# Kernel tuning notes

Hardware: AMD Instinct MI355X
Metric: run time of the kernel (lower is better)

## Reference

```python
import jax, jax.numpy as jnp
import numpy as np

NF = 256  # node_feat_size
GF = 256  # graph_feat_size
V = 262144
G = 4096


def setup_inputs() -> dict:
    key = jax.random.key(0)
    ks = jax.random.split(key, 12)
    node_feats = jax.random.normal(ks[0], (V, NF), dtype=jnp.float32)
    g_feats = jax.random.normal(ks[1], (G, GF), dtype=jnp.float32)
    segment_ids = jnp.sort(jax.random.randint(ks[2], (V,), 0, G, dtype=jnp.int32))
    s = 0.05
    # compute_logits: Linear(NF+GF -> 1)
    Wl = jax.random.normal(ks[3], (1, NF + GF), dtype=jnp.float32) * s
    bl = jnp.zeros((1,), dtype=jnp.float32)
    # project_nodes: Linear(NF -> GF)  (dropout=0 -> identity)
    Wp = jax.random.normal(ks[4], (GF, NF), dtype=jnp.float32) * s
    bp = jnp.zeros((GF,), dtype=jnp.float32)
    # GRUCell(GF, GF), torch gate order (r, z, n)
    W_ih = jax.random.normal(ks[5], (3 * GF, GF), dtype=jnp.float32) * s
    W_hh = jax.random.normal(ks[6], (3 * GF, GF), dtype=jnp.float32) * s
    b_ih = jnp.zeros((3 * GF,), dtype=jnp.float32)
    b_hh = jnp.zeros((3 * GF,), dtype=jnp.float32)
    return dict(node_feats=node_feats, g_feats=g_feats, segment_ids=segment_ids,
                Wl=Wl, bl=bl, Wp=Wp, bp=bp,
                W_ih=W_ih, W_hh=W_hh, b_ih=b_ih, b_hh=b_hh)


def reference(node_feats, g_feats, segment_ids, Wl, bl, Wp, bp, W_ih, W_hh, b_ih, b_hh):
    num_graphs = g_feats.shape[0]
    # broadcast relu(g_feats) to nodes, concat with node feats, logits Linear + LeakyReLU
    gb = jax.nn.relu(g_feats)[segment_ids]                      # [V, GF]
    cat = jnp.concatenate([gb, node_feats], axis=1)             # [V, GF+NF]
    z = jax.nn.leaky_relu(cat @ Wl.T + bl, negative_slope=0.01) # [V, 1]
    # segmented softmax over nodes per graph
    m = jax.ops.segment_max(z, segment_ids, num_segments=num_graphs,
                            indices_are_sorted=True)            # [G, 1]
    e = jnp.exp(z - m[segment_ids])                             # [V, 1]
    denom = jax.ops.segment_sum(e, segment_ids, num_segments=num_graphs,
                                indices_are_sorted=True)        # [G, 1]
    a = e / denom[segment_ids]                                  # [V, 1]
    # project nodes (dropout p=0 -> identity) and weighted sum per graph
    hv = node_feats @ Wp.T + bp                                 # [V, GF]
    context = jax.ops.segment_sum(a * hv, segment_ids, num_segments=num_graphs,
                                  indices_are_sorted=True)      # [G, GF]
    context = jax.nn.elu(context)
    # GRUCell: input=context, hidden=g_feats, torch gate order r,z,n
    gi = context @ W_ih.T + b_ih                                # [G, 3*GF]
    gh = g_feats @ W_hh.T + b_hh                                # [G, 3*GF]
    i_r, i_z, i_n = jnp.split(gi, 3, axis=1)
    h_r, h_z, h_n = jnp.split(gh, 3, axis=1)
    r = jax.nn.sigmoid(i_r + h_r)
    u = jax.nn.sigmoid(i_z + h_z)
    n = jnp.tanh(i_n + r * h_n)
    h_new = (1.0 - u) * n + u * g_feats
    return h_new
```

## Files before the change

### kernel.cpp

```cpp
#include <hip/hip_runtime.h>
#include <hip/hip_bf16.h>
#include <stdint.h>

typedef unsigned short u16;
typedef __attribute__((ext_vector_type(8))) short short8;
typedef __attribute__((ext_vector_type(4))) float floatx4;

#define NFEAT 256

__device__ __forceinline__ unsigned short f2b(float f) {
    unsigned int x = __builtin_bit_cast(unsigned int, f);
    x += 0x7fffu + ((x >> 16) & 1u);
    return (unsigned short)(x >> 16);
}
__device__ __forceinline__ float sigmoidf_(float x) {
    return 1.0f / (1.0f + __expf(-x));
}

__global__ void __launch_bounds__(256)
k1_attn_pool(const float* __restrict__ nf, const float* __restrict__ gf,
             const int* __restrict__ seg, const float* __restrict__ Wl,
             const float* __restrict__ bl,
             const float* __restrict__ Wp, const float* __restrict__ Wih,
             const float* __restrict__ Whh,
             u16* __restrict__ s_out,
             float* __restrict__ pres, u16* __restrict__ gfb,
             u16* __restrict__ wpb, u16* __restrict__ wihb, u16* __restrict__ whhb,
             int V)
{
    const int g = blockIdx.x;
    const int t = threadIdx.x;
    __shared__ float red[256];
    __shared__ float accs[4][256];
    __shared__ float mws[4], lws[4];

    {
        const int n1 = 256 * 256;
        const int n2 = n1 + 768 * 256;
        const int n3 = n2 + 768 * 256;
        int idx = g * 256 + t;
        if (idx < n3) {
            if (idx < n1)       wpb[idx]       = f2b(Wp[idx]);
            else if (idx < n2)  wihb[idx - n1] = f2b(Wih[idx - n1]);
            else                whhb[idx - n2] = f2b(Whh[idx - n2]);
        }
    }

    const float gfv = gf[(size_t)g * NFEAT + t];
    gfb[(size_t)g * NFEAT + t] = f2b(gfv);
    red[t] = fmaxf(gfv, 0.0f) * Wl[t];
    __syncthreads();
    #pragma unroll
    for (int off = 128; off > 0; off >>= 1) {
        if (t < off) red[t] += red[t + off];
        __syncthreads();
    }
    const float gbase = red[0] + bl[0];
    __syncthreads();

    int lo = 0, hi = V;
    while (lo < hi) { int mid = (lo + hi) >> 1; if (seg[mid] < g) lo = mid + 1; else hi = mid; }
    const int start = lo;
    hi = V;
    while (lo < hi) { int mid = (lo + hi) >> 1; if (seg[mid] <= g) lo = mid + 1; else hi = mid; }
    const int count = lo - start;

    const int lane = t & 63;
    const int wv = t >> 6;

    const float4 wn = *(const float4*)(Wl + NFEAT + lane * 4);

    float m = -3.0e38f, l = 0.0f;
    float4 acc = {0.f, 0.f, 0.f, 0.f};
    const float* base = nf + (size_t)start * NFEAT + lane * 4;

    float4 x = {0.f, 0.f, 0.f, 0.f};
    if (wv < count) x = *(const float4*)(base + (size_t)wv * NFEAT);
    for (int i = wv; i < count; i += 4) {
        float4 nx = {0.f, 0.f, 0.f, 0.f};
        if (i + 4 < count) nx = *(const float4*)(base + (size_t)(i + 4) * NFEAT);
        float d = x.x * wn.x + x.y * wn.y + x.z * wn.z + x.w * wn.w;
        #pragma unroll
        for (int off = 32; off > 0; off >>= 1) d += __shfl_xor(d, off);
        float z = d + gbase;
        z = (z > 0.0f) ? z : 0.01f * z;
        float mn = fmaxf(m, z);
        float c = __expf(m - mn);
        float p = __expf(z - mn);
        l = l * c + p;
        acc.x = acc.x * c + p * x.x;
        acc.y = acc.y * c + p * x.y;
        acc.z = acc.z * c + p * x.z;
        acc.w = acc.w * c + p * x.w;
        m = mn;
        x = nx;
    }

    accs[wv][lane * 4 + 0] = acc.x;
    accs[wv][lane * 4 + 1] = acc.y;
    accs[wv][lane * 4 + 2] = acc.z;
    accs[wv][lane * 4 + 3] = acc.w;
    if (lane == 0) { mws[wv] = m; lws[wv] = l; }
    __syncthreads();

    const float M = fmaxf(fmaxf(mws[0], mws[1]), fmaxf(mws[2], mws[3]));
    const float c0 = __expf(mws[0] - M), c1 = __expf(mws[1] - M);
    const float c2 = __expf(mws[2] - M), c3 = __expf(mws[3] - M);
    const float L = lws[0] * c0 + lws[1] * c1 + lws[2] * c2 + lws[3] * c3;
    const float sv = accs[0][t] * c0 + accs[1][t] * c1 + accs[2][t] * c2 + accs[3][t] * c3;
    const float inv = (L > 0.0f) ? 1.0f / L : 0.0f;
    s_out[(size_t)g * NFEAT + t] = f2b(sv * inv);
    if (t == 0) pres[g] = (count > 0) ? 1.0f : 0.0f;
}

__global__ void __launch_bounds__(256)
k2a_project(const u16* __restrict__ s, const u16* __restrict__ Wpb,
            const float* __restrict__ bp, const float* __restrict__ pres,
            u16* __restrict__ ctx)
{
    const int t = threadIdx.x;
    const int wid = blockIdx.x * 4 + (t >> 6);
    const int lane = t & 63;
    const int m0 = (wid >> 4) * 16;
    const int n0 = (wid & 15) * 16;
    const int lr = lane & 15;
    const int kh = lane >> 4;

    const short* A = (const short*)s   + (size_t)(m0 + lr) * NFEAT + kh * 8;
    const short* B = (const short*)Wpb + (size_t)(n0 + lr) * NFEAT + kh * 8;

    floatx4 acc = {0.f, 0.f, 0.f, 0.f};
    #pragma unroll
    for (int k = 0; k < NFEAT; k += 32) {
        short8 a = *(const short8*)(A + k);
        short8 b = *(const short8*)(B + k);
        acc = __builtin_amdgcn_mfma_f32_16x16x32_bf16(a, b, acc, 0, 0, 0);
    }
    const int col = n0 + lr;
    const float bias = bp[col];
    const int rbase = m0 + kh * 4;
    #pragma unroll
    for (int r = 0; r < 4; ++r) {
        int row = rbase + r;
        float x = acc[r] + bias * pres[row];
        x = (x > 0.0f) ? x : (__expf(x) - 1.0f);
        ctx[(size_t)row * NFEAT + col] = f2b(x);
    }
}

__global__ void __launch_bounds__(256)
k2b_gru(const u16* __restrict__ ctx, const u16* __restrict__ gfb,
        const float* __restrict__ gf,
        const u16* __restrict__ Wih, const u16* __restrict__ Whh,
        const float* __restrict__ bih, const float* __restrict__ bhh,
        float* __restrict__ out)
{
    const int t = threadIdx.x;
    const int wid = blockIdx.x * 4 + (t >> 6);
    const int lane = t & 63;
    const int m0 = (wid >> 4) * 16;
    const int j0 = (wid & 15) * 16;
    const int lr = lane & 15;
    const int kh = lane >> 4;

    const short* A1 = (const short*)ctx + (size_t)(m0 + lr) * NFEAT + kh * 8;
    const short* A2 = (const short*)gfb + (size_t)(m0 + lr) * NFEAT + kh * 8;
    const size_t boff = (size_t)(j0 + lr) * NFEAT + kh * 8;
    const short* Bir = (const short*)Wih + boff;
    const short* Biz = Bir + 256 * NFEAT;
    const short* Bin = Bir + 512 * NFEAT;
    const short* Bhr = (const short*)Whh + boff;
    const short* Bhz = Bhr + 256 * NFEAT;
    const short* Bhn = Bhr + 512 * NFEAT;

    floatx4 air = {0,0,0,0}, aiz = {0,0,0,0}, ain = {0,0,0,0};
    floatx4 ahr = {0,0,0,0}, ahz = {0,0,0,0}, ahn = {0,0,0,0};
    #pragma unroll
    for (int k = 0; k < NFEAT; k += 32) {
        short8 a1 = *(const short8*)(A1 + k);
        short8 a2 = *(const short8*)(A2 + k);
        air = __builtin_amdgcn_mfma_f32_16x16x32_bf16(a1, *(const short8*)(Bir + k), air, 0, 0, 0);
        aiz = __builtin_amdgcn_mfma_f32_16x16x32_bf16(a1, *(const short8*)(Biz + k), aiz, 0, 0, 0);
        ain = __builtin_amdgcn_mfma_f32_16x16x32_bf16(a1, *(const short8*)(Bin + k), ain, 0, 0, 0);
        ahr = __builtin_amdgcn_mfma_f32_16x16x32_bf16(a2, *(const short8*)(Bhr + k), ahr, 0, 0, 0);
        ahz = __builtin_amdgcn_mfma_f32_16x16x32_bf16(a2, *(const short8*)(Bhz + k), ahz, 0, 0, 0);
        ahn = __builtin_amdgcn_mfma_f32_16x16x32_bf16(a2, *(const short8*)(Bhn + k), ahn, 0, 0, 0);
    }
    const int col = j0 + lr;
    const float b_ir = bih[col], b_iz = bih[256 + col], b_in = bih[512 + col];
    const float b_hr = bhh[col], b_hz = bhh[256 + col], b_hn = bhh[512 + col];
    const int rbase = m0 + kh * 4;
    #pragma unroll
    for (int r = 0; r < 4; ++r) {
        int row = rbase + r;
        float rg = sigmoidf_((air[r] + b_ir) + (ahr[r] + b_hr));
        float ug = sigmoidf_((aiz[r] + b_iz) + (ahz[r] + b_hz));
        float ng = tanhf((ain[r] + b_in) + rg * (ahn[r] + b_hn));
        float h  = gf[(size_t)row * NFEAT + col];
        out[(size_t)row * NFEAT + col] = (1.0f - ug) * ng + ug * h;
    }
}

extern "C" void kernel_launch(void* const* d_in, const int* in_sizes, int n_in,
                              void* d_out, int out_size, void* d_ws, size_t ws_size,
                              hipStream_t stream)
{
    const float* nf  = (const float*)d_in[0];
    const float* gf  = (const float*)d_in[1];
    const int*   seg = (const int*)d_in[2];
    const float* Wl  = (const float*)d_in[3];
    const float* bl  = (const float*)d_in[4];
    const float* Wp  = (const float*)d_in[5];
    const float* bp  = (const float*)d_in[6];
    const float* Wih = (const float*)d_in[7];
    const float* Whh = (const float*)d_in[8];
    const float* bih = (const float*)d_in[9];
    const float* bhh = (const float*)d_in[10];

    const int V = in_sizes[2];
    const int G = in_sizes[1] / NFEAT;

    char* ws = (char*)d_ws;
    u16*   sbuf = (u16*)ws;                           ws += (size_t)G * NFEAT * 2;
    u16*   ctx  = (u16*)ws;                           ws += (size_t)G * NFEAT * 2;
    u16*   gfb  = (u16*)ws;                           ws += (size_t)G * NFEAT * 2;
    u16*   wpb  = (u16*)ws;                           ws += (size_t)256 * 256 * 2;
    u16*   wihb = (u16*)ws;                           ws += (size_t)768 * 256 * 2;
    u16*   whhb = (u16*)ws;                           ws += (size_t)768 * 256 * 2;
    float* pres = (float*)ws;                         ws += (size_t)G * 4;

    k1_attn_pool<<<G, 256, 0, stream>>>(nf, gf, seg, Wl, bl, Wp, Wih, Whh,
                                        sbuf, pres, gfb, wpb, wihb, whhb, V);
    k2a_project<<<G / 4, 256, 0, stream>>>(sbuf, wpb, bp, pres, ctx);
    k2b_gru<<<G / 4, 256, 0, stream>>>(ctx, gfb, gf, wihb, whhb, bih, bhh, (float*)d_out);
    (void)ws_size; (void)n_in; (void)out_size;
}
```

Before: 438.1 us.

## Fuse projection and GRU kernels via LDS context; unroll pooling loop by two nodes

Merges the projection+ELU kernel and the GRU kernel into one 512-thread kernel per 16 graphs. The context tile stays in shared memory instead of round-tripping through global memory, and A fragments are kept in registers and reused across two output tiles per wave. Separately, the attention-pooling loop now handles two nodes per wave per iteration, which raises memory-level parallelism in the dominant streaming pass. The cost is higher register pressure and fewer blocks in the fused GEMM stage.

```diff
diff --git a/kernel.cpp b/kernel.cpp
--- a/kernel.cpp
+++ b/kernel.cpp
@@ -74,26 +74,39 @@
     float4 acc = {0.f, 0.f, 0.f, 0.f};
     const float* base = nf + (size_t)start * NFEAT + lane * 4;
 
-    float4 x = {0.f, 0.f, 0.f, 0.f};
-    if (wv < count) x = *(const float4*)(base + (size_t)wv * NFEAT);
-    for (int i = wv; i < count; i += 4) {
-        float4 nx = {0.f, 0.f, 0.f, 0.f};
-        if (i + 4 < count) nx = *(const float4*)(base + (size_t)(i + 4) * NFEAT);
-        float d = x.x * wn.x + x.y * wn.y + x.z * wn.z + x.w * wn.w;
-        #pragma unroll
-        for (int off = 32; off > 0; off >>= 1) d += __shfl_xor(d, off);
-        float z = d + gbase;
-        z = (z > 0.0f) ? z : 0.01f * z;
-        float mn = fmaxf(m, z);
-        float c = __expf(m - mn);
-        float p = __expf(z - mn);
-        l = l * c + p;
-        acc.x = acc.x * c + p * x.x;
-        acc.y = acc.y * c + p * x.y;
-        acc.z = acc.z * c + p * x.z;
-        acc.w = acc.w * c + p * x.w;
+    float4 x0 = {0.f,0.f,0.f,0.f}, x1 = {0.f,0.f,0.f,0.f};
+    {
+        int i = wv * 2;
+        if (i < count)     x0 = *(const float4*)(base + (size_t)i * NFEAT);
+        if (i + 1 < count) x1 = *(const float4*)(base + (size_t)(i + 1) * NFEAT);
+    }
+    for (int i = wv * 2; i < count; i += 8) {
+        float4 p0v = {0.f,0.f,0.f,0.f}, p1v = {0.f,0.f,0.f,0.f};
+        if (i + 8 < count) p0v = *(const float4*)(base + (size_t)(i + 8) * NFEAT);
+        if (i + 9 < count) p1v = *(const float4*)(base + (size_t)(i + 9) * NFEAT);
+
+        float d0 = x0.x * wn.x + x0.y * wn.y + x0.z * wn.z + x0.w * wn.w;
+        float d1 = x1.x * wn.x + x1.y * wn.y + x1.z * wn.z + x1.w * wn.w;
+        #pragma unroll
+        for (int off = 32; off > 0; off >>= 1) {
+            d0 += __shfl_xor(d0, off);
+            d1 += __shfl_xor(d1, off);
+        }
+        float z0 = d0 + gbase; z0 = (z0 > 0.0f) ? z0 : 0.01f * z0;
+        float z1 = d1 + gbase; z1 = (z1 > 0.0f) ? z1 : 0.01f * z1;
+        if (i + 1 >= count) z1 = -3.0e38f;
+
+        float mn = fmaxf(m, fmaxf(z0, z1));
+        float c  = __expf(m - mn);
+        float p0 = __expf(z0 - mn);
+        float p1 = __expf(z1 - mn);
+        l = l * c + p0 + p1;
+        acc.x = acc.x * c + p0 * x0.x + p1 * x1.x;
+        acc.y = acc.y * c + p0 * x0.y + p1 * x1.y;
+        acc.z = acc.z * c + p0 * x0.z + p1 * x1.z;
+        acc.w = acc.w * c + p0 * x0.w + p1 * x1.w;
         m = mn;
-        x = nx;
+        x0 = p0v; x1 = p1v;
     }
 
     accs[wv][lane * 4 + 0] = acc.x;
@@ -113,91 +126,95 @@
     if (t == 0) pres[g] = (count > 0) ? 1.0f : 0.0f;
 }
 
-__global__ void __launch_bounds__(256)
-k2a_project(const u16* __restrict__ s, const u16* __restrict__ Wpb,
-            const float* __restrict__ bp, const float* __restrict__ pres,
-            u16* __restrict__ ctx)
+#define CTX_LD 264
+__global__ void __launch_bounds__(512)
+k2_fused(const u16* __restrict__ s, const u16* __restrict__ wpb,
+         const float* __restrict__ bp, const float* __restrict__ pres,
+         const u16* __restrict__ gfb, const float* __restrict__ gf,
+         const u16* __restrict__ wihb, const u16* __restrict__ whhb,
+         const float* __restrict__ bih, const float* __restrict__ bhh,
+         float* __restrict__ out)
 {
+    __shared__ u16 ctx[16][CTX_LD];
     const int t = threadIdx.x;
-    const int wid = blockIdx.x * 4 + (t >> 6);
+    const int w = t >> 6;
     const int lane = t & 63;
-    const int m0 = (wid >> 4) * 16;
-    const int n0 = (wid & 15) * 16;
+    const int m0 = blockIdx.x * 16;
     const int lr = lane & 15;
     const int kh = lane >> 4;
 
-    const short* A = (const short*)s   + (size_t)(m0 + lr) * NFEAT + kh * 8;
-    const short* B = (const short*)Wpb + (size_t)(n0 + lr) * NFEAT + kh * 8;
-
-    floatx4 acc = {0.f, 0.f, 0.f, 0.f};
+    {
+        const short* A = (const short*)s + (size_t)(m0 + lr) * NFEAT + kh * 8;
+        short8 af[8];
+        #pragma unroll
+        for (int kk = 0; kk < 8; ++kk) af[kk] = *(const short8*)(A + kk * 32);
+
+        #pragma unroll
+        for (int nt = 0; nt < 2; ++nt) {
+            const int n0 = (w * 2 + nt) * 16;
+            const short* B = (const short*)wpb + (size_t)(n0 + lr) * NFEAT + kh * 8;
+            floatx4 acc = {0.f, 0.f, 0.f, 0.f};
+            #pragma unroll
+            for (int kk = 0; kk < 8; ++kk)
+                acc = __builtin_amdgcn_mfma_f32_16x16x32_bf16(af[kk], *(const short8*)(B + kk * 32), acc, 0, 0, 0);
+            const int col = n0 + lr;
+            const float bias = bp[col];
+            #pragma unroll
+            for (int r = 0; r < 4; ++r) {
+                int rl = kh * 4 + r;
+                float x = acc[r] + bias * pres[m0 + rl];
+                x = (x > 0.0f) ? x : (__expf(x) - 1.0f);
+                ctx[rl][col] = f2b(x);
+            }
+        }
+    }
+    __syncthreads();
+
+    short8 a1[8], a2[8];
     #pragma unroll
-    for (int k = 0; k < NFEAT; k += 32) {
-        short8 a = *(const short8*)(A + k);
-        short8 b = *(const short8*)(B + k);
-        acc = __builtin_amdgcn_mfma_f32_16x16x32_bf16(a, b, acc, 0, 0, 0);
-    }
-    const int col = n0 + lr;
-    const float bias = bp[col];
-    const int rbase = m0 + kh * 4;
+    for (int kk = 0; kk < 8; ++kk)
+        a1[kk] = *(const short8*)&ctx[lr][kk * 32 + kh * 8];
+    {
+        const short* A2 = (const short*)gfb + (size_t)(m0 + lr) * NFEAT + kh * 8;
+        #pragma unroll
+        for (int kk = 0; kk < 8; ++kk) a2[kk] = *(const short8*)(A2 + kk * 32);
+    }
+
     #pragma unroll
-    for (int r = 0; r < 4; ++r) {
-        int row = rbase + r;
-        float x = acc[r] + bias * pres[row];
-        x = (x > 0.0f) ? x : (__expf(x) - 1.0f);
-        ctx[(size_t)row * NFEAT + col] = f2b(x);
-    }
-}
-
-__global__ void __launch_bounds__(256)
-k2b_gru(const u16* __restrict__ ctx, const u16* __restrict__ gfb,
-        const float* __restrict__ gf,
-        const u16* __restrict__ Wih, const u16* __restrict__ Whh,
-        const float* __restrict__ bih, const float* __restrict__ bhh,
-        float* __restrict__ out)
-{
-    const int t = threadIdx.x;
-    const int wid = blockIdx.x * 4 + (t >> 6);
-    const int lane = t & 63;
-    const int m0 = (wid >> 4) * 16;
-    const int j0 = (wid & 15) * 16;
-    const int lr = lane & 15;
-    const int kh = lane >> 4;
-
-    const short* A1 = (const short*)ctx + (size_t)(m0 + lr) * NFEAT + kh * 8;
-    const short* A2 = (const short*)gfb + (size_t)(m0 + lr) * NFEAT + kh * 8;
-    const size_t boff = (size_t)(j0 + lr) * NFEAT + kh * 8;
-    const short* Bir = (const short*)Wih + boff;
-    const short* Biz = Bir + 256 * NFEAT;
-    const short* Bin = Bir + 512 * NFEAT;
-    const short* Bhr = (const short*)Whh + boff;
-    const short* Bhz = Bhr + 256 * NFEAT;
-    const short* Bhn = Bhr + 512 * NFEAT;
-
-    floatx4 air = {0,0,0,0}, aiz = {0,0,0,0}, ain = {0,0,0,0};
-    floatx4 ahr = {0,0,0,0}, ahz = {0,0,0,0}, ahn = {0,0,0,0};
-    #pragma unroll
-    for (int k = 0; k < NFEAT; k += 32) {
-        short8 a1 = *(const short8*)(A1 + k);
-        short8 a2 = *(const short8*)(A2 + k);
-        air = __builtin_amdgcn_mfma_f32_16x16x32_bf16(a1, *(const short8*)(Bir + k), air, 0, 0, 0);
-        aiz = __builtin_amdgcn_mfma_f32_16x16x32_bf16(a1, *(const short8*)(Biz + k), aiz, 0, 0, 0);
-        ain = __builtin_amdgcn_mfma_f32_16x16x32_bf16(a1, *(const short8*)(Bin + k), ain, 0, 0, 0);
-        ahr = __builtin_amdgcn_mfma_f32_16x16x32_bf16(a2, *(const short8*)(Bhr + k), ahr, 0, 0, 0);
-        ahz = __builtin_amdgcn_mfma_f32_16x16x32_bf16(a2, *(const short8*)(Bhz + k), ahz, 0, 0, 0);
-        ahn = __builtin_amdgcn_mfma_f32_16x16x32_bf16(a2, *(const short8*)(Bhn + k), ahn, 0, 0, 0);
-    }
-    const int col = j0 + lr;
-    const float b_ir = bih[col], b_iz = bih[256 + col], b_in = bih[512 + col];
-    const float b_hr = bhh[col], b_hz = bhh[256 + col], b_hn = bhh[512 + col];
-    const int rbase = m0 + kh * 4;
-    #pragma unroll
-    for (int r = 0; r < 4; ++r) {
-        int row = rbase + r;
-        float rg = sigmoidf_((air[r] + b_ir) + (ahr[r] + b_hr));
-        float ug = sigmoidf_((aiz[r] + b_iz) + (ahz[r] + b_hz));
-        float ng = tanhf((ain[r] + b_in) + rg * (ahn[r] + b_hn));
-        float h  = gf[(size_t)row * NFEAT + col];
-        out[(size_t)row * NFEAT + col] = (1.0f - ug) * ng + ug * h;
+    for (int jt = 0; jt < 2; ++jt) {
+        const int j0 = (w * 2 + jt) * 16;
+        const size_t boff = (size_t)(j0 + lr) * NFEAT + kh * 8;
+        const short* Bir = (const short*)wihb + boff;
+        const short* Biz = Bir + 256 * NFEAT;
+        const short* Bin = Bir + 512 * NFEAT;
+        const short* Bhr = (const short*)whhb + boff;
+        const short* Bhz = Bhr + 256 * NFEAT;
+        const short* Bhn = Bhr + 512 * NFEAT;
+
+        floatx4 air = {0,0,0,0}, aiz = {0,0,0,0}, ain = {0,0,0,0};
+        floatx4 ahr = {0,0,0,0}, ahz = {0,0,0,0}, ahn = {0,0,0,0};
+        #pragma unroll
+        for (int kk = 0; kk < 8; ++kk) {
+            const int k = kk * 32;
+            air = __builtin_amdgcn_mfma_f32_16x16x32_bf16(a1[kk], *(const short8*)(Bir + k), air, 0, 0, 0);
+            aiz = __builtin_amdgcn_mfma_f32_16x16x32_bf16(a1[kk], *(const short8*)(Biz + k), aiz, 0, 0, 0);
+            ain = __builtin_amdgcn_mfma_f32_16x16x32_bf16(a1[kk], *(const short8*)(Bin + k), ain, 0, 0, 0);
+            ahr = __builtin_amdgcn_mfma_f32_16x16x32_bf16(a2[kk], *(const short8*)(Bhr + k), ahr, 0, 0, 0);
+            ahz = __builtin_amdgcn_mfma_f32_16x16x32_bf16(a2[kk], *(const short8*)(Bhz + k), ahz, 0, 0, 0);
+            ahn = __builtin_amdgcn_mfma_f32_16x16x32_bf16(a2[kk], *(const short8*)(Bhn + k), ahn, 0, 0, 0);
+        }
+        const int col = j0 + lr;
+        const float b_ir = bih[col], b_iz = bih[256 + col], b_in = bih[512 + col];
+        const float b_hr = bhh[col], b_hz = bhh[256 + col], b_hn = bhh[512 + col];
+        #pragma unroll
+        for (int r = 0; r < 4; ++r) {
+            int row = m0 + kh * 4 + r;
+            float rg = sigmoidf_((air[r] + b_ir) + (ahr[r] + b_hr));
+            float ug = sigmoidf_((aiz[r] + b_iz) + (ahz[r] + b_hz));
+            float ng = tanhf((ain[r] + b_in) + rg * (ahn[r] + b_hn));
+            float h  = gf[(size_t)row * NFEAT + col];
+            out[(size_t)row * NFEAT + col] = (1.0f - ug) * ng + ug * h;
+        }
     }
 }
 
@@ -222,7 +239,6 @@
 
     char* ws = (char*)d_ws;
     u16*   sbuf = (u16*)ws;                           ws += (size_t)G * NFEAT * 2;
-    u16*   ctx  = (u16*)ws;                           ws += (size_t)G * NFEAT * 2;
     u16*   gfb  = (u16*)ws;                           ws += (size_t)G * NFEAT * 2;
     u16*   wpb  = (u16*)ws;                           ws += (size_t)256 * 256 * 2;
     u16*   wihb = (u16*)ws;                           ws += (size_t)768 * 256 * 2;
@@ -231,7 +247,7 @@
 
     k1_attn_pool<<<G, 256, 0, stream>>>(nf, gf, seg, Wl, bl, Wp, Wih, Whh,
                                         sbuf, pres, gfb, wpb, wihb, whhb, V);
-    k2a_project<<<G / 4, 256, 0, stream>>>(sbuf, wpb, bp, pres, ctx);
-    k2b_gru<<<G / 4, 256, 0, stream>>>(ctx, gfb, gf, wihb, whhb, bih, bhh, (float*)d_out);
+    k2_fused<<<G / 16, 512, 0, stream>>>(sbuf, wpb, bp, pres, gfb, gf,
+                                         wihb, whhb, bih, bhh, (float*)d_out);
     (void)ws_size; (void)n_in; (void)out_size;
 }
```

Result: faster. 427.1 us (-2.5%).
